# Performance work log

Hardware: AMD Instinct MI355X
Metric: run time of the kernel (lower is better)

## Reference

```python
import jax, jax.numpy as jnp
import numpy as np

B, T, E = 64, 512, 128
NODES, PATHS, OUT = 100000, 200000, 1000
PAD = 1  # padding_idx for node embedding


def setup_inputs() -> dict:
    key = jax.random.key(0)
    ks = jax.random.split(key, 10)
    starts = jax.random.randint(ks[0], (B, T), 0, NODES)
    paths = jax.random.randint(ks[1], (B, T), 0, PATHS)
    ends = jax.random.randint(ks[2], (B, T), 0, NODES)
    length = jax.random.randint(ks[3], (B,), 0, T)
    node_emb = jax.random.normal(ks[4], (NODES, E), dtype=jnp.float32)
    path_emb = jax.random.normal(ks[5], (PATHS, E), dtype=jnp.float32)
    W = jax.random.normal(ks[6], (E, 3 * E), dtype=jnp.float32)
    a = jax.random.normal(ks[7], (E,), dtype=jnp.float32)
    out_W = jax.random.normal(ks[8], (OUT, E), dtype=jnp.float32) * (1.0 / np.sqrt(E))
    out_b = jax.random.normal(ks[9], (OUT,), dtype=jnp.float32) * 0.01
    return dict(starts=starts, paths=paths, ends=ends, length=length,
                node_emb=node_emb, path_emb=path_emb, W=W, a=a,
                out_W=out_W, out_b=out_b)


def reference(starts, paths, ends, length, node_emb, path_emb, W, a, out_W, out_b):
    # padding_idx=1 -> that embedding row is zero
    node_emb = node_emb.at[PAD].set(0.0)
    es = node_emb[starts]          # [B,T,E]
    ep = path_emb[paths]           # [B,T,E]
    ee = node_emb[ends]            # [B,T,E]
    c = jnp.concatenate([es, ep, ee], axis=2)          # [B,T,3E]
    # dropout is identity in eval mode
    x = jnp.tanh(jnp.einsum('ed,btd->bte', W, c))      # [B,T,E]
    z = jax.nn.softmax(x @ a, axis=1)                  # [B,T] softmax over full T
    # original code sums only first length[i] attention weights (no renorm)
    mask = (jnp.arange(T)[None, :] < length[:, None]).astype(x.dtype)  # [B,T]
    v = jnp.einsum('bte,bt->be', x, z * mask)          # [B,E]
    return v @ out_W.T + out_b                          # [B,OUT]
```

## Files before the change

kernel.cpp:

```cpp
#include <hip/hip_runtime.h>

#define BB     64
#define TT     512
#define EE     128
#define NROWS  (BB * TT)
#define PADIDX 1
#define OUTN   1000

typedef __attribute__((ext_vector_type(8)))  short short8;
typedef __attribute__((ext_vector_type(16))) float f32x16;

__device__ __forceinline__ float tanh_fast(float v) {
    return 1.0f - 2.0f / (__expf(2.0f * v) + 1.0f);
}

__device__ __forceinline__ void split8(float4 a0, float4 a1, short8& hi, short8& lo) {
    float f[8] = {a0.x, a0.y, a0.z, a0.w, a1.x, a1.y, a1.z, a1.w};
#pragma unroll
    for (int i = 0; i < 8; ++i) {
        unsigned u = __float_as_uint(f[i]);
        unsigned r = (u + (0x7fffu + ((u >> 16) & 1u))) & 0xffff0000u;
        hi[i] = (short)(r >> 16);
        lo[i] = (short)(__float_as_uint(f[i] - __uint_as_float(r)) >> 16);
    }
}

__global__ __launch_bounds__(256)
void k_prep(const float* __restrict__ W, unsigned short* __restrict__ Whg,
            unsigned short* __restrict__ Wlg)
{
    const int id = blockIdx.x * 256 + threadIdx.x;
    const int j  = id & 7;
    const int l  = (id >> 3) & 63;
    const int r2 = id >> 9;
    const int ks = r2 % 24;
    const int et = r2 / 24;
    const int e  = et * 32 + (l & 31);
    const int k  = ks * 16 + (l >> 5) * 8 + j;

    const float v = W[e * 384 + k];
    unsigned u = __float_as_uint(v);
    unsigned r = (u + (0x7fffu + ((u >> 16) & 1u))) & 0xffff0000u;
    Whg[id] = (unsigned short)(r >> 16);
    Wlg[id] = (unsigned short)(__float_as_uint(v - __uint_as_float(r)) >> 16);
}

__global__ __launch_bounds__(256, 2)
void k_gemm_x(const int* __restrict__ starts, const int* __restrict__ paths,
              const int* __restrict__ ends,
              const float* __restrict__ node_emb, const float* __restrict__ path_emb,
              const unsigned short* __restrict__ Whg, const unsigned short* __restrict__ Wlg,
              const float* __restrict__ a, float* __restrict__ x, float* __restrict__ s)
{
    __shared__ float s_red[64][4];

    const int tid  = threadIdx.x;
    const int lane = tid & 63;
    const int w    = tid >> 6;
    const int fr   = lane & 31;
    const int kh   = lane >> 5;
    const int r0   = blockIdx.x * 64;

    const char* base[2][3];
    bool padf[2][3];
#pragma unroll
    for (int mi = 0; mi < 2; ++mi) {
        const int row = r0 + mi * 32 + fr;
        const int i0 = starts[row], i1 = paths[row], i2 = ends[row];
        base[mi][0] = (const char*)node_emb + (size_t)i0 * 512 + kh * 32;
        base[mi][1] = (const char*)path_emb + (size_t)i1 * 512 + kh * 32;
        base[mi][2] = (const char*)node_emb + (size_t)i2 * 512 + kh * 32;
        padf[mi][0] = (i0 == PADIDX);
        padf[mi][1] = false;
        padf[mi][2] = (i2 == PADIDX);
    }

    const char* wbh = (const char*)Whg + ((size_t)(w * 24 * 64) + lane) * 16;
    const char* wbl = (const char*)Wlg + ((size_t)(w * 24 * 64) + lane) * 16;

    f32x16 acc[2];
#pragma unroll
    for (int mi = 0; mi < 2; ++mi)
#pragma unroll
        for (int i = 0; i < 16; ++i) acc[mi][i] = 0.0f;

#pragma unroll
    for (int ks = 0; ks < 24; ++ks) {
        const int seg = ks >> 3;
        const int off = (ks & 7) * 64;

        const short8 bh = *(const short8*)(wbh + ks * 1024);
        const short8 bl = *(const short8*)(wbl + ks * 1024);

        float4 a0[2], a1[2];
#pragma unroll
        for (int mi = 0; mi < 2; ++mi) {
            a0[mi] = *(const float4*)(base[mi][seg] + off);
            a1[mi] = *(const float4*)(base[mi][seg] + off + 16);
            if (padf[mi][seg]) {
                a0[mi] = make_float4(0.f, 0.f, 0.f, 0.f);
                a1[mi] = a0[mi];
            }
        }
#pragma unroll
        for (int mi = 0; mi < 2; ++mi) {
            short8 ah, al;
            split8(a0[mi], a1[mi], ah, al);
            acc[mi] = __builtin_amdgcn_mfma_f32_32x32x16_bf16(ah, bh, acc[mi], 0, 0, 0);
            acc[mi] = __builtin_amdgcn_mfma_f32_32x32x16_bf16(ah, bl, acc[mi], 0, 0, 0);
            acc[mi] = __builtin_amdgcn_mfma_f32_32x32x16_bf16(al, bh, acc[mi], 0, 0, 0);
        }
    }

    const float av = a[w * 32 + fr];

#pragma unroll
    for (int mi = 0; mi < 2; ++mi) {
        float sp[16];
#pragma unroll
        for (int r = 0; r < 16; ++r) {
            const int rowl = (r & 3) + 8 * (r >> 2) + 4 * kh;
            const float tv = tanh_fast(acc[mi][r]);
            x[(size_t)(r0 + mi * 32 + rowl) * EE + w * 32 + fr] = tv;
            sp[r] = tv * av;
        }
#pragma unroll
        for (int m = 1; m < 32; m <<= 1)
#pragma unroll
            for (int r = 0; r < 16; ++r) sp[r] += __shfl_xor(sp[r], m, 64);
        if (fr == 0) {
#pragma unroll
            for (int r = 0; r < 16; ++r) {
                const int rowl = (r & 3) + 8 * (r >> 2) + 4 * kh;
                s_red[mi * 32 + rowl][w] = sp[r];
            }
        }
    }
    __syncthreads();
    if (tid < 64)
        s[r0 + tid] = s_red[tid][0] + s_red[tid][1] + s_red[tid][2] + s_red[tid][3];
}

__global__ __launch_bounds__(256)
void k_attn(const float* __restrict__ s, const int* __restrict__ length,
            const float* __restrict__ x, float* __restrict__ v)
{
    __shared__ float sw[TT];
    __shared__ float red[256];

    const int b   = blockIdx.x >> 2;
    const int ec  = blockIdx.x & 3;
    const int tid = threadIdx.x;

    const float s0 = s[b * TT + tid];
    const float s1 = s[b * TT + 256 + tid];

    red[tid] = fmaxf(s0, s1);
    __syncthreads();
    for (int st = 128; st > 0; st >>= 1) {
        if (tid < st) red[tid] = fmaxf(red[tid], red[tid + st]);
        __syncthreads();
    }
    const float mx = red[0];
    __syncthreads();

    const float e0 = __expf(s0 - mx);
    const float e1 = __expf(s1 - mx);
    red[tid] = e0 + e1;
    __syncthreads();
    for (int st = 128; st > 0; st >>= 1) {
        if (tid < st) red[tid] += red[tid + st];
        __syncthreads();
    }
    const float inv = 1.0f / red[0];
    const int   len = length[b];
    __syncthreads();

    sw[tid]       = e0 * inv;
    sw[tid + 256] = e1 * inv;
    __syncthreads();

    const int e  = ec * 32 + (tid & 31);
    const int tp = tid >> 5;
    const float* xb = x + (size_t)b * TT * EE;
    float acc = 0.0f;
    for (int t = tp; t < len; t += 8)
        acc = fmaf(sw[t], xb[(size_t)t * EE + e], acc);

    red[tid] = acc;
    __syncthreads();
    if (tid < 32) {
        float r2 = 0.0f;
#pragma unroll
        for (int k = 0; k < 8; ++k) r2 += red[k * 32 + tid];
        v[b * EE + ec * 32 + tid] = r2;
    }
}

__global__ __launch_bounds__(256)
void k_out(const float* __restrict__ v, const float* __restrict__ out_W,
           const float* __restrict__ out_b, float* __restrict__ out)
{
    const int id = blockIdx.x * 256 + threadIdx.x;
    const int o  = id >> 6;
    const int bb = id & 63;

    const float4* vr = (const float4*)(v + bb * EE);
    const float4* wr = (const float4*)(out_W + o * EE);
    float acc = 0.0f;
#pragma unroll 8
    for (int qq = 0; qq < 32; ++qq) {
        const float4 a4 = vr[qq];
        const float4 b4 = wr[qq];
        acc = fmaf(a4.x, b4.x, acc);
        acc = fmaf(a4.y, b4.y, acc);
        acc = fmaf(a4.z, b4.z, acc);
        acc = fmaf(a4.w, b4.w, acc);
    }
    out[bb * OUTN + o] = acc + out_b[o];
}

extern "C" void kernel_launch(void* const* d_in, const int* in_sizes, int n_in,
                              void* d_out, int out_size, void* d_ws, size_t ws_size,
                              hipStream_t stream)
{
    const int*   starts   = (const int*)d_in[0];
    const int*   paths    = (const int*)d_in[1];
    const int*   ends     = (const int*)d_in[2];
    const int*   length   = (const int*)d_in[3];
    const float* node_emb = (const float*)d_in[4];
    const float* path_emb = (const float*)d_in[5];
    const float* W        = (const float*)d_in[6];
    const float* a        = (const float*)d_in[7];
    const float* out_W    = (const float*)d_in[8];
    const float* out_b    = (const float*)d_in[9];
    float*       out      = (float*)d_out;

    float* x = (float*)d_ws;
    float* s = x + (size_t)NROWS * EE;
    float* v = s + NROWS;
    unsigned short* Whg = (unsigned short*)(v + BB * EE);
    unsigned short* Wlg = Whg + 49152;

    k_prep<<<192, 256, 0, stream>>>(W, Whg, Wlg);
    k_gemm_x<<<NROWS / 64, 256, 0, stream>>>(starts, paths, ends,
                                             node_emb, path_emb, Whg, Wlg,
                                             a, x, s);
    k_attn<<<BB * 4, 256, 0, stream>>>(s, length, x, v);
    k_out<<<(BB * OUTN) / 256, 256, 0, stream>>>(v, out_W, out_b, out);
}
```

Measured before the change: 225.2 us.

## Repartition gemm_x waves into M-by-split-K tiles with register double-buffered loads

```diff
diff --git a/kernel.cpp b/kernel.cpp
--- a/kernel.cpp
+++ b/kernel.cpp
@@ -52,93 +52,126 @@
               const unsigned short* __restrict__ Whg, const unsigned short* __restrict__ Wlg,
               const float* __restrict__ a, float* __restrict__ x, float* __restrict__ s)
 {
-    __shared__ float s_red[64][4];
+    __shared__ float mrg[64 * 128];
 
     const int tid  = threadIdx.x;
     const int lane = tid & 63;
     const int w    = tid >> 6;
+    const int mg   = w >> 1;
+    const int kg   = w & 1;
     const int fr   = lane & 31;
     const int kh   = lane >> 5;
     const int r0   = blockIdx.x * 64;
 
-    const char* base[2][3];
-    bool padf[2][3];
-#pragma unroll
-    for (int mi = 0; mi < 2; ++mi) {
-        const int row = r0 + mi * 32 + fr;
-        const int i0 = starts[row], i1 = paths[row], i2 = ends[row];
-        base[mi][0] = (const char*)node_emb + (size_t)i0 * 512 + kh * 32;
-        base[mi][1] = (const char*)path_emb + (size_t)i1 * 512 + kh * 32;
-        base[mi][2] = (const char*)node_emb + (size_t)i2 * 512 + kh * 32;
-        padf[mi][0] = (i0 == PADIDX);
-        padf[mi][1] = false;
-        padf[mi][2] = (i2 == PADIDX);
-    }
-
-    const char* wbh = (const char*)Whg + ((size_t)(w * 24 * 64) + lane) * 16;
-    const char* wbl = (const char*)Wlg + ((size_t)(w * 24 * 64) + lane) * 16;
-
-    f32x16 acc[2];
-#pragma unroll
-    for (int mi = 0; mi < 2; ++mi)
-#pragma unroll
-        for (int i = 0; i < 16; ++i) acc[mi][i] = 0.0f;
-
-#pragma unroll
-    for (int ks = 0; ks < 24; ++ks) {
-        const int seg = ks >> 3;
-        const int off = (ks & 7) * 64;
-
-        const short8 bh = *(const short8*)(wbh + ks * 1024);
-        const short8 bl = *(const short8*)(wbl + ks * 1024);
-
-        float4 a0[2], a1[2];
-#pragma unroll
-        for (int mi = 0; mi < 2; ++mi) {
-            a0[mi] = *(const float4*)(base[mi][seg] + off);
-            a1[mi] = *(const float4*)(base[mi][seg] + off + 16);
-            if (padf[mi][seg]) {
-                a0[mi] = make_float4(0.f, 0.f, 0.f, 0.f);
-                a1[mi] = a0[mi];
+    const int row = r0 + mg * 32 + fr;
+    const int i0 = starts[row], i1 = paths[row], i2 = ends[row];
+    const char* baseA0 = (const char*)node_emb + (size_t)i0 * 512 + kh * 32;
+    const char* baseA1 = (const char*)path_emb + (size_t)i1 * 512 + kh * 32;
+    const char* baseA2 = (const char*)node_emb + (size_t)i2 * 512 + kh * 32;
+    const bool pad0 = (i0 == PADIDX), pad2 = (i2 == PADIDX);
+
+    const char* pbh = (const char*)Whg + lane * 16;
+    const char* pbl = (const char*)Wlg + lane * 16;
+
+    f32x16 acc[4];
+#pragma unroll
+    for (int ni = 0; ni < 4; ++ni)
+#pragma unroll
+        for (int i = 0; i < 16; ++i) acc[ni][i] = 0.0f;
+
+    float4 a0b[2], a1b[2];
+    short8 bhb[2][4], blb[2][4];
+
+#define ISSUE_A(SLOT, KS) do {                                                  \
+    const int seg_ = (KS) >> 3;                                                 \
+    const char* p_ = (seg_ == 0 ? baseA0 : (seg_ == 1 ? baseA1 : baseA2))       \
+                   + ((KS) & 7) * 64;                                           \
+    a0b[SLOT] = *(const float4*)p_;                                             \
+    a1b[SLOT] = *(const float4*)(p_ + 16);                                      \
+} while (0)
+
+#define ISSUE_B(SLOT, KS) do {                                                  \
+    _Pragma("unroll")                                                           \
+    for (int ni_ = 0; ni_ < 4; ++ni_) {                                         \
+        bhb[SLOT][ni_] = *(const short8*)(pbh + ni_ * 24576 + (KS) * 1024);     \
+        blb[SLOT][ni_] = *(const short8*)(pbl + ni_ * 24576 + (KS) * 1024);     \
+    }                                                                           \
+} while (0)
+
+#define KLOOP(KS0) do {                                                         \
+    ISSUE_A(0, (KS0));  ISSUE_A(1, (KS0) + 1);  ISSUE_B(0, (KS0));              \
+    _Pragma("unroll")                                                           \
+    for (int j = 0; j < 12; ++j) {                                              \
+        const int seg_c = ((KS0) + j) >> 3;                                     \
+        float4 ca0 = a0b[j & 1], ca1 = a1b[j & 1];                              \
+        const bool pad_ = (seg_c == 0) ? pad0 : ((seg_c == 2) ? pad2 : false);  \
+        if (pad_) { ca0 = make_float4(0.f, 0.f, 0.f, 0.f); ca1 = ca0; }         \
+        if (j + 2 < 12) ISSUE_A(j & 1, (KS0) + j + 2);                          \
+        if (j + 1 < 12) ISSUE_B((j + 1) & 1, (KS0) + j + 1);                    \
+        short8 ah, al;                                                          \
+        split8(ca0, ca1, ah, al);                                               \
+        _Pragma("unroll")                                                       \
+        for (int ni = 0; ni < 4; ++ni) {                                        \
+            acc[ni] = __builtin_amdgcn_mfma_f32_32x32x16_bf16(ah, bhb[j & 1][ni], acc[ni], 0, 0, 0); \
+            acc[ni] = __builtin_amdgcn_mfma_f32_32x32x16_bf16(ah, blb[j & 1][ni], acc[ni], 0, 0, 0); \
+            acc[ni] = __builtin_amdgcn_mfma_f32_32x32x16_bf16(al, bhb[j & 1][ni], acc[ni], 0, 0, 0); \
+        }                                                                       \
+    }                                                                           \
+} while (0)
+
+    if (kg == 0) KLOOP(0); else KLOOP(12);
+
+#undef ISSUE_A
+#undef ISSUE_B
+#undef KLOOP
+
+    if (kg == 1) {
+#pragma unroll
+        for (int ni = 0; ni < 4; ++ni)
+#pragma unroll
+            for (int r = 0; r < 16; ++r)
+                mrg[(ni * 16 + r) * 128 + mg * 64 + lane] = acc[ni][r];
+    }
+    __syncthreads();
+
+    if (kg == 0) {
+#pragma unroll
+        for (int ni = 0; ni < 4; ++ni)
+#pragma unroll
+            for (int r = 0; r < 16; ++r)
+                acc[ni][r] += mrg[(ni * 16 + r) * 128 + mg * 64 + lane];
+
+        float av[4];
+#pragma unroll
+        for (int ni = 0; ni < 4; ++ni) av[ni] = a[ni * 32 + fr];
+
+        float sp[16];
+#pragma unroll
+        for (int r = 0; r < 16; ++r) sp[r] = 0.0f;
+
+#pragma unroll
+        for (int ni = 0; ni < 4; ++ni)
+#pragma unroll
+            for (int r = 0; r < 16; ++r) {
+                const int rowl = (r & 3) + 8 * (r >> 2) + 4 * kh;
+                const float tv = tanh_fast(acc[ni][r]);
+                x[(size_t)(r0 + mg * 32 + rowl) * EE + ni * 32 + fr] = tv;
+                sp[r] = fmaf(tv, av[ni], sp[r]);
+            }
+
+#pragma unroll
+        for (int m = 1; m < 32; m <<= 1)
+#pragma unroll
+            for (int r = 0; r < 16; ++r) sp[r] += __shfl_xor(sp[r], m, 64);
+
+        if (fr == 0) {
+#pragma unroll
+            for (int r = 0; r < 16; ++r) {
+                const int rowl = (r & 3) + 8 * (r >> 2) + 4 * kh;
+                s[r0 + mg * 32 + rowl] = sp[r];
             }
         }
-#pragma unroll
-        for (int mi = 0; mi < 2; ++mi) {
-            short8 ah, al;
-            split8(a0[mi], a1[mi], ah, al);
-            acc[mi] = __builtin_amdgcn_mfma_f32_32x32x16_bf16(ah, bh, acc[mi], 0, 0, 0);
-            acc[mi] = __builtin_amdgcn_mfma_f32_32x32x16_bf16(ah, bl, acc[mi], 0, 0, 0);
-            acc[mi] = __builtin_amdgcn_mfma_f32_32x32x16_bf16(al, bh, acc[mi], 0, 0, 0);
-        }
-    }
-
-    const float av = a[w * 32 + fr];
-
-#pragma unroll
-    for (int mi = 0; mi < 2; ++mi) {
-        float sp[16];
-#pragma unroll
-        for (int r = 0; r < 16; ++r) {
-            const int rowl = (r & 3) + 8 * (r >> 2) + 4 * kh;
-            const float tv = tanh_fast(acc[mi][r]);
-            x[(size_t)(r0 + mi * 32 + rowl) * EE + w * 32 + fr] = tv;
-            sp[r] = tv * av;
-        }
-#pragma unroll
-        for (int m = 1; m < 32; m <<= 1)
-#pragma unroll
-            for (int r = 0; r < 16; ++r) sp[r] += __shfl_xor(sp[r], m, 64);
-        if (fr == 0) {
-#pragma unroll
-            for (int r = 0; r < 16; ++r) {
-                const int rowl = (r & 3) + 8 * (r >> 2) + 4 * kh;
-                s_red[mi * 32 + rowl][w] = sp[r];
-            }
-        }
-    }
-    __syncthreads();
-    if (tid < 64)
-        s[r0 + tid] = s_red[tid][0] + s_red[tid][1] + s_red[tid][2] + s_red[tid][3];
+    }
 }
 
 __global__ __launch_bounds__(256)
```

After: 219.9 us. 2.3% less time.
